# Kernel tuning notes

Hardware: AMD Instinct MI355X
Metric: run time of the kernel (lower is better)

The kernel has to match this reference:

```python
import jax, jax.numpy as jnp
import numpy as np

B, N, F = 2, 3000, 64
H, OUT, ATT = 4, 16, 16
DENSITY = 0.01


def setup_inputs() -> dict:
    key = jax.random.key(0)
    ks = jax.random.split(key, 6)
    h = jax.random.normal(ks[0], (B, N, F), dtype=jnp.float32)
    a = (jax.random.uniform(ks[1], (B, N, N)) < DENSITY).astype(jnp.float32)
    glorot = lambda k, shape: jax.random.uniform(
        k, shape, jnp.float32, -1.0, 1.0) * jnp.sqrt(6.0 / (shape[-2] + shape[-1]))
    kernel = glorot(ks[2], (H, F, OUT))
    attention_kernel = glorot(ks[3], (H, F, ATT))
    attention_kernel_2 = glorot(ks[4], (H, F, ATT))
    bias = jax.random.normal(ks[5], (1, 1, H, OUT), dtype=jnp.float32) * 0.01
    return {"h": h, "a": a, "kernel": kernel,
            "attention_kernel": attention_kernel,
            "attention_kernel_2": attention_kernel_2, "bias": bias}


def reference(h, a, kernel, attention_kernel, attention_kernel_2, bias):
    # h: [B,N,F], a: [B,N,N] dense binary adjacency
    feats = jnp.einsum('bnf,hfo->bhno', h, kernel)            # [B,H,N,OUT]
    f_self = jnp.einsum('bnf,hfd->hbnd', h, attention_kernel)   # [H,B,N,A]
    f_other = jnp.einsum('bnf,hfd->hbdn', h, attention_kernel_2)  # [H,B,A,N]
    a_h = a[None]                                               # [1,B,N,N] broadcast over heads
    scores = jnp.einsum('hbnd,hbdm->hbnm', f_self, f_other)     # [H,B,N,N]
    masked = a_h * scores
    masked = jnp.where(masked >= 0, masked, 0.2 * masked)       # LeakyReLU(0.2)
    masked = masked / jnp.sqrt(jnp.float32(ATT))
    masked = masked + jnp.where(a_h == 0, jnp.float32(-1e9), jnp.float32(0.0))
    attn = jax.nn.softmax(masked, axis=-1)
    attn = attn * jnp.where(a_h == 0, jnp.float32(0.0), jnp.float32(1.0))
    attn = jnp.transpose(attn, (1, 0, 2, 3))                    # [B,H,N,N]
    # dropout_rate=0 / inference -> identity
    node_features = jnp.einsum('bhnm,bhmo->bhno', attn, feats)  # [B,H,N,OUT]
    node_features = node_features + jnp.transpose(bias, (0, 2, 1, 3))  # [1,H,1,OUT]
    node_features = jax.nn.relu(node_features)
    node_features = jnp.transpose(node_features, (0, 2, 1, 3))  # [B,N,H,OUT]
    return node_features.reshape(-1, N, H * OUT)
```

## Files before the change

kernel.cpp:

```cpp
#include <hip/hip_runtime.h>
#include <math.h>

#define B_   2
#define N_   3000
#define F_   64
#define H_   4
#define O_   16
#define HO_  64
#define MAXD 64
#define NF4  750
#define NN   (B_*N_)
#define NPB  12

typedef float f32x4 __attribute__((ext_vector_type(4)));
typedef float f32x2 __attribute__((ext_vector_type(2)));

template<int CTRL>
__device__ __forceinline__ float ror_add(float x) {
    const int r = __builtin_amdgcn_update_dpp(0, __float_as_int(x), CTRL, 0xF, 0xF, true);
    return x + __int_as_float(r);
}
__device__ __forceinline__ float seg16_sum(float x) {
    x = ror_add<0x121>(x);
    x = ror_add<0x122>(x);
    x = ror_add<0x124>(x);
    x = ror_add<0x128>(x);
    return x;
}

__global__ __launch_bounds__(192) void proj_kernel(
    const float* __restrict__ h,
    const float* __restrict__ K,
    const float* __restrict__ AK,
    const float* __restrict__ AK2,
    float* __restrict__ combI,
    float* __restrict__ fs)
{
    const int tid  = threadIdx.x;
    const int m    = tid >> 6;
    const int lane = tid & 63;
    const int nbase = blockIdx.x * NPB;

    __shared__ float4 hrow[NPB][16];

    {
        const int j  = tid >> 4;
        const int f4 = tid & 15;
        hrow[j][f4] = ((const float4*)(h + (size_t)(nbase + j) * F_))[f4];
    }

    const float* Wm = (m == 0) ? AK2 : (m == 1) ? K : AK;
    const float* Wc = Wm + ((lane >> 4) << 10) + (lane & 15);
    f32x4 w4[16];
#pragma unroll
    for (int f4 = 0; f4 < 16; ++f4) {
        w4[f4][0] = Wc[(f4 * 4 + 0) << 4];
        w4[f4][1] = Wc[(f4 * 4 + 1) << 4];
        w4[f4][2] = Wc[(f4 * 4 + 2) << 4];
        w4[f4][3] = Wc[(f4 * 4 + 3) << 4];
    }
    __syncthreads();

#pragma unroll
    for (int j = 0; j < NPB; ++j) {
        float a0 = 0.f, a1 = 0.f, a2 = 0.f, a3 = 0.f;
#pragma unroll
        for (int f4 = 0; f4 < 16; ++f4) {
            const float4 hv = hrow[j][f4];
            a0 = fmaf(hv.x, w4[f4][0], a0);
            a1 = fmaf(hv.y, w4[f4][1], a1);
            a2 = fmaf(hv.z, w4[f4][2], a2);
            a3 = fmaf(hv.w, w4[f4][3], a3);
        }
        const float av = (a0 + a1) + (a2 + a3);
        const int node = nbase + j;
        if (m == 0)      combI[(size_t)node * 128 + lane * 2 + 0] = av;
        else if (m == 1) combI[(size_t)node * 128 + lane * 2 + 1] = av;
        else             fs   [(size_t)node * HO_ + lane]         = av;
    }
}

__global__ __launch_bounds__(256, 4) void gat_wave_kernel(
    const float* __restrict__ a,
    const float* __restrict__ combI,
    const float* __restrict__ fs,
    const float* __restrict__ bias,
    float* __restrict__ out)
{
    const int tid  = threadIdx.x;
    const int w    = tid >> 6;
    const int lane = tid & 63;
    const int row  = blockIdx.x * 4 + w;
    const int b    = row / N_;
    const int bbase = b * N_;

    __shared__ int nbr[4][MAXD];

    const float biasv = bias[lane];
    const float fsv   = fs[(size_t)row * HO_ + lane];

    const f32x4* arow = (const f32x4*)(a + (size_t)row * N_);
    unsigned long long msk = 0ull;
#pragma unroll
    for (int g = 0; g < 2; ++g) {
        f32x4 v[6];
#pragma unroll
        for (int it = 0; it < 6; ++it) {
            const int c4 = (g * 6 + it) * 64 + lane;
            v[it] = (f32x4)(0.f);
            if (c4 < NF4) v[it] = __builtin_nontemporal_load(arow + c4);
        }
#pragma unroll
        for (int it = 0; it < 6; ++it) {
            const unsigned int nib = (unsigned int)(v[it][0] != 0.f)
                                   | ((unsigned int)(v[it][1] != 0.f) << 1)
                                   | ((unsigned int)(v[it][2] != 0.f) << 2)
                                   | ((unsigned int)(v[it][3] != 0.f) << 3);
            msk |= ((unsigned long long)nib) << ((g * 6 + it) * 4);
        }
    }

    const int c = __popcll(msk);
    int incl = c;
#pragma unroll
    for (int d = 1; d < 64; d <<= 1) {
        const int t = __shfl_up(incl, d);
        if (lane >= d) incl += t;
    }
    int tot = __shfl(incl, 63);
    if (tot > MAXD) tot = MAXD;
    {
        unsigned long long m2 = msk;
        int k = incl - c;
        while (m2 && k < MAXD) {
            const int bpos = __builtin_ctzll(m2);
            m2 &= m2 - 1ull;
            nbr[w][k] = ((bpos >> 2) << 8) + (lane << 2) + (bpos & 3);
            ++k;
        }
    }
    asm volatile("s_waitcnt lgkmcnt(0)" ::: "memory");
    int nid = nbr[w][lane];
    nid = (lane < tot) ? nid : 0;

    float acc = 0.f, sum = 0.f;
#define BATCH16(B0)                                                             \
    {                                                                           \
        f32x2 v[16];                                                            \
        _Pragma("unroll")                                                       \
        for (int k = 0; k < 16; ++k) {                                          \
            const int mm = __builtin_amdgcn_readlane(nid, (B0) + k);            \
            const f32x2* bp = (const f32x2*)(combI + ((size_t)(bbase + mm) << 7)); \
            v[k] = bp[lane];                        \
        }                                                                       \
        _Pragma("unroll")                                                       \
        for (int k = 0; k < 16; ++k) {                                          \
            const float sdot = seg16_sum(fsv * v[k][0]);                        \
            const float tt = (sdot >= 0.f ? sdot : 0.2f * sdot) * 0.25f;        \
            const float e = ((B0) + k < tot) ? __expf(tt) : 0.f;                \
            acc = fmaf(e, v[k][1], acc);                                        \
            sum += e;                                                           \
        }                                                                       \
    }
    BATCH16(0);
    if (tot > 16) BATCH16(16);
    if (tot > 32) {
        BATCH16(32);
        if (tot > 48) BATCH16(48);
    }
#undef BATCH16

    const float inv = (tot > 0) ? 1.f / sum : 0.f;
    out[(size_t)row * HO_ + lane] = fmaxf(fmaf(acc, inv, biasv), 0.f);
}

extern "C" void kernel_launch(void* const* d_in, const int* in_sizes, int n_in,
                              void* d_out, int out_size, void* d_ws, size_t ws_size,
                              hipStream_t stream) {
    const float* h    = (const float*)d_in[0];
    const float* a    = (const float*)d_in[1];
    const float* K    = (const float*)d_in[2];
    const float* AK   = (const float*)d_in[3];
    const float* AK2  = (const float*)d_in[4];
    const float* bias = (const float*)d_in[5];
    float* out = (float*)d_out;

    float* combI = (float*)d_ws;
    float* fs    = combI + (size_t)NN * 128;

    hipLaunchKernelGGL(proj_kernel, dim3(NN / NPB), dim3(192), 0, stream,
                       h, K, AK, AK2, combI, fs);
    hipLaunchKernelGGL(gat_wave_kernel, dim3(NN / 4), dim3(256), 0, stream,
                       a, combI, fs, bias, out);
}
```

Baseline: 35.80 us.

## Process four adjacency rows per single wavefront to raise memory-level parallelism

The attention kernel now launches one 64-thread wavefront per block, and each wavefront handles four rows instead of one. Adjacency loads for all four rows are issued together, the prefix scans are interleaved, and neighbour gathers are batched in groups of eight across rows. This is meant to give each wave more independent memory requests in flight and hide gather latency. In exchange it raises register pressure (24 float4 loads live at once) and leaves fewer waves resident, which could reduce occupancy.

```diff
diff --git a/kernel.cpp b/kernel.cpp
--- a/kernel.cpp
+++ b/kernel.cpp
@@ -80,98 +80,123 @@
     }
 }
 
-__global__ __launch_bounds__(256, 4) void gat_wave_kernel(
+__global__ __launch_bounds__(64) void gat4_kernel(
     const float* __restrict__ a,
     const float* __restrict__ combI,
     const float* __restrict__ fs,
     const float* __restrict__ bias,
     float* __restrict__ out)
 {
-    const int tid  = threadIdx.x;
-    const int w    = tid >> 6;
-    const int lane = tid & 63;
-    const int row  = blockIdx.x * 4 + w;
-    const int b    = row / N_;
-    const int bbase = b * N_;
+    const int lane = threadIdx.x;
+    const int r0   = blockIdx.x * 4;
+    const int bbase = (r0 >= N_) ? N_ : 0;
 
     __shared__ int nbr[4][MAXD];
 
     const float biasv = bias[lane];
-    const float fsv   = fs[(size_t)row * HO_ + lane];
-
-    const f32x4* arow = (const f32x4*)(a + (size_t)row * N_);
-    unsigned long long msk = 0ull;
+    float fsv[4];
+#pragma unroll
+    for (int r = 0; r < 4; ++r) fsv[r] = fs[(size_t)(r0 + r) * HO_ + lane];
+
+    unsigned long long mk[4] = {0ull, 0ull, 0ull, 0ull};
 #pragma unroll
     for (int g = 0; g < 2; ++g) {
-        f32x4 v[6];
-#pragma unroll
-        for (int it = 0; it < 6; ++it) {
-            const int c4 = (g * 6 + it) * 64 + lane;
-            v[it] = (f32x4)(0.f);
-            if (c4 < NF4) v[it] = __builtin_nontemporal_load(arow + c4);
-        }
-#pragma unroll
-        for (int it = 0; it < 6; ++it) {
-            const unsigned int nib = (unsigned int)(v[it][0] != 0.f)
-                                   | ((unsigned int)(v[it][1] != 0.f) << 1)
-                                   | ((unsigned int)(v[it][2] != 0.f) << 2)
-                                   | ((unsigned int)(v[it][3] != 0.f) << 3);
-            msk |= ((unsigned long long)nib) << ((g * 6 + it) * 4);
-        }
-    }
-
-    const int c = __popcll(msk);
-    int incl = c;
+        f32x4 sv[4][6];
+#pragma unroll
+        for (int r = 0; r < 4; ++r) {
+            const f32x4* arow = (const f32x4*)(a + (size_t)(r0 + r) * N_);
+#pragma unroll
+            for (int it = 0; it < 6; ++it) {
+                const int c4 = (g * 6 + it) * 64 + lane;
+                sv[r][it] = (f32x4)(0.f);
+                if (c4 < NF4) sv[r][it] = __builtin_nontemporal_load(arow + c4);
+            }
+        }
+#pragma unroll
+        for (int r = 0; r < 4; ++r) {
+#pragma unroll
+            for (int it = 0; it < 6; ++it) {
+                const unsigned int nib = (unsigned int)(sv[r][it][0] != 0.f)
+                                       | ((unsigned int)(sv[r][it][1] != 0.f) << 1)
+                                       | ((unsigned int)(sv[r][it][2] != 0.f) << 2)
+                                       | ((unsigned int)(sv[r][it][3] != 0.f) << 3);
+                mk[r] |= ((unsigned long long)nib) << ((g * 6 + it) * 4);
+            }
+        }
+    }
+
+    int cnt[4], incl[4], tot[4];
+#pragma unroll
+    for (int r = 0; r < 4; ++r) { cnt[r] = __popcll(mk[r]); incl[r] = cnt[r]; }
 #pragma unroll
     for (int d = 1; d < 64; d <<= 1) {
-        const int t = __shfl_up(incl, d);
-        if (lane >= d) incl += t;
-    }
-    int tot = __shfl(incl, 63);
-    if (tot > MAXD) tot = MAXD;
-    {
-        unsigned long long m2 = msk;
-        int k = incl - c;
+#pragma unroll
+        for (int r = 0; r < 4; ++r) {
+            const int t = __shfl_up(incl[r], d);
+            if (lane >= d) incl[r] += t;
+        }
+    }
+#pragma unroll
+    for (int r = 0; r < 4; ++r) {
+        tot[r] = __shfl(incl[r], 63);
+        if (tot[r] > MAXD) tot[r] = MAXD;
+    }
+#pragma unroll
+    for (int r = 0; r < 4; ++r) {
+        unsigned long long m2 = mk[r];
+        int k = incl[r] - cnt[r];
         while (m2 && k < MAXD) {
             const int bpos = __builtin_ctzll(m2);
             m2 &= m2 - 1ull;
-            nbr[w][k] = ((bpos >> 2) << 8) + (lane << 2) + (bpos & 3);
+            nbr[r][k] = ((bpos >> 2) << 8) + (lane << 2) + (bpos & 3);
             ++k;
         }
     }
     asm volatile("s_waitcnt lgkmcnt(0)" ::: "memory");
-    int nid = nbr[w][lane];
-    nid = (lane < tot) ? nid : 0;
-
-    float acc = 0.f, sum = 0.f;
-#define BATCH16(B0)                                                             \
-    {                                                                           \
-        f32x2 v[16];                                                            \
-        _Pragma("unroll")                                                       \
-        for (int k = 0; k < 16; ++k) {                                          \
-            const int mm = __builtin_amdgcn_readlane(nid, (B0) + k);            \
-            const f32x2* bp = (const f32x2*)(combI + ((size_t)(bbase + mm) << 7)); \
-            v[k] = bp[lane];                        \
-        }                                                                       \
-        _Pragma("unroll")                                                       \
-        for (int k = 0; k < 16; ++k) {                                          \
-            const float sdot = seg16_sum(fsv * v[k][0]);                        \
-            const float tt = (sdot >= 0.f ? sdot : 0.2f * sdot) * 0.25f;        \
-            const float e = ((B0) + k < tot) ? __expf(tt) : 0.f;                \
-            acc = fmaf(e, v[k][1], acc);                                        \
-            sum += e;                                                           \
-        }                                                                       \
-    }
-    BATCH16(0);
-    if (tot > 16) BATCH16(16);
-    if (tot > 32) {
-        BATCH16(32);
-        if (tot > 48) BATCH16(48);
-    }
-#undef BATCH16
-
-    const float inv = (tot > 0) ? 1.f / sum : 0.f;
-    out[(size_t)row * HO_ + lane] = fmaxf(fmaf(acc, inv, biasv), 0.f);
+    int nid[4];
+#pragma unroll
+    for (int r = 0; r < 4; ++r) {
+        nid[r] = nbr[r][lane];
+        nid[r] = (lane < tot[r]) ? nid[r] : 0;
+    }
+
+    float acc[4] = {0.f, 0.f, 0.f, 0.f};
+    float sum[4] = {0.f, 0.f, 0.f, 0.f};
+#pragma unroll
+    for (int b = 0; b < 8; ++b) {
+        f32x2 gv[4][8];
+#pragma unroll
+        for (int r = 0; r < 4; ++r) {
+            if (tot[r] > b * 8) {
+#pragma unroll
+                for (int k = 0; k < 8; ++k) {
+                    const int mm = __builtin_amdgcn_readlane(nid[r], b * 8 + k);
+                    const f32x2* bp =
+                        (const f32x2*)(combI + ((size_t)(bbase + mm) << 7));
+                    gv[r][k] = bp[lane];
+                }
+            }
+        }
+#pragma unroll
+        for (int r = 0; r < 4; ++r) {
+            if (tot[r] > b * 8) {
+#pragma unroll
+                for (int k = 0; k < 8; ++k) {
+                    const float sdot = seg16_sum(fsv[r] * gv[r][k][0]);
+                    const float tt = (sdot >= 0.f ? sdot : 0.2f * sdot) * 0.25f;
+                    const float e = (b * 8 + k < tot[r]) ? __expf(tt) : 0.f;
+                    acc[r] = fmaf(e, gv[r][k][1], acc[r]);
+                    sum[r] += e;
+                }
+            }
+        }
+    }
+
+#pragma unroll
+    for (int r = 0; r < 4; ++r) {
+        const float inv = (tot[r] > 0) ? 1.f / sum[r] : 0.f;
+        out[(size_t)(r0 + r) * HO_ + lane] = fmaxf(fmaf(acc[r], inv, biasv), 0.f);
+    }
 }
 
 extern "C" void kernel_launch(void* const* d_in, const int* in_sizes, int n_in,
@@ -190,6 +215,6 @@
 
     hipLaunchKernelGGL(proj_kernel, dim3(NN / NPB), dim3(192), 0, stream,
                        h, K, AK, AK2, combI, fs);
-    hipLaunchKernelGGL(gat_wave_kernel, dim3(NN / 4), dim3(256), 0, stream,
+    hipLaunchKernelGGL(gat4_kernel, dim3(NN / 4), dim3(64), 0, stream,
                        a, combI, fs, bias, out);
 }
```

Result: slower. 44.98 us (+25.6%).
